# Optimization experiments

Measured on AMD Instinct MI355X. Metric: run time of the kernel, lower is better.

Reference implementation:

```python
import jax, jax.numpy as jnp
import numpy as np

GAMMA = 4  # channel groups (s)


def setup_inputs() -> dict:
    key = jax.random.key(0)
    k1, k2, k3, k4 = jax.random.split(key, 4)
    b, w, n, c = 16, 128, 256, 128  # batch, windows, win_size, channels
    x = jax.random.normal(k1, (b, w, n, c), dtype=jnp.float32)
    att_std = 0.01
    attention_centers = att_std * jax.random.normal(k2, (GAMMA, 1), dtype=jnp.float32)
    attention_spreads = 1.0 + att_std * jax.random.normal(k3, (GAMMA, 1), dtype=jnp.float32)
    token_proj_n_bias = 0.01 * jax.random.normal(k4, (1, n, 1), dtype=jnp.float32)
    return {"x": x, "attention_centers": attention_centers,
            "attention_spreads": attention_spreads,
            "token_proj_n_bias": token_proj_n_bias}


def _rel_indices(n):
    idx = jnp.arange(n, dtype=jnp.float32)
    d = idx[None, :] - idx[:, None]          # (n, n)
    return jnp.stack([d, d * d], axis=-1)     # (n, n, 2): [indx, indx^2]


def reference(x, attention_centers, attention_spreads, token_proj_n_bias):
    b, w, n, c = x.shape
    s = attention_centers.shape[0]
    v = c // s
    # pos_proj = -1/2 * [-2*delta*inv_cov, inv_cov]  -> (s, 2)
    pos_proj = -0.5 * jnp.concatenate(
        [-2.0 * attention_centers * attention_spreads, attention_spreads], axis=-1)
    rel = _rel_indices(n)                                   # (n, n, 2)
    pos_score = jnp.einsum('mnd,sd->mns', rel, pos_proj)    # (m, n, s)
    posmap = jax.nn.softmax(pos_score, axis=1)              # softmax over n
    xr = x.reshape(b, w, n, v, s)
    out = jnp.einsum('mns,bwnvs->bwmvs', posmap, xr)        # contract tokens n
    out = out + token_proj_n_bias[None, :, :, :, None]       # (1,1,n,1,1) broadcast
    return out.reshape(b, w, n, c)
```

## Files before the change

kernel.cpp:

```cpp
#include <hip/hip_runtime.h>
#include <hip/hip_bf16.h>


#define N_TOK 256
#define C_CH  128
#define NV    32
#define HW    8
#define TAPS  17
#define PMPAD 18
#define MCHUNK 64
#define ROWS  (MCHUNK + 2*HW)
#define XFL4  (ROWS * NV)
#define PMFL4 (MCHUNK * PMPAD)

typedef const __attribute__((address_space(1))) void gvoid_t;
typedef __attribute__((address_space(3))) void       lvoid_t;

__global__ void pm_build_kernel(const float* __restrict__ centers,
                                const float* __restrict__ spreads,
                                float* __restrict__ pmb) {
    const int m    = blockIdx.x;
    const int lane = threadIdx.x;
    const int n    = m + lane - HW;
    const bool valid = (lane < TAPS) && ((unsigned)n < N_TOK);
    const float dd = (float)(lane - HW);

    float e[4];
#pragma unroll
    for (int s = 0; s < 4; ++s) {
        const float ctr = centers[s];
        const float spr = spreads[s];
        const float sc = (ctr * spr) * dd - 0.5f * spr * dd * dd;
        e[s] = valid ? expf(sc) : 0.0f;
    }
#pragma unroll
    for (int s = 0; s < 4; ++s) {
        float v = e[s];
#pragma unroll
        for (int off = 32; off; off >>= 1) v += __shfl_xor(v, off, 64);
        e[s] = e[s] / __shfl(v, 0, 64);
    }
    if (lane < PMPAD) {
        reinterpret_cast<float4*>(pmb)[m * PMPAD + lane] =
            make_float4(e[0], e[1], e[2], e[3]);
    }
}

__global__ __launch_bounds__(256, 2)
void pm_apply_kernel(const float* __restrict__ x,
                     const float* __restrict__ pmb,
                     const float* __restrict__ bias,
                     float* __restrict__ out) {
    const int m0   = blockIdx.x * MCHUNK;
    const int bw   = blockIdx.y;
    const int row0 = m0 - HW;
    const int tid  = threadIdx.x;

    __shared__ float4 lds_x[XFL4];
    __shared__ float4 lds_pm[PMFL4];

    const float* xb = x + (size_t)bw * (N_TOK * C_CH);

#pragma unroll
    for (int i = 0; i < XFL4 / 256; ++i) {
        const int idx = tid + i * 256;
        const int r = idx >> 5;
        const int v = idx & 31;
        int n = row0 + r;
        n = n < 0 ? 0 : (n > N_TOK - 1 ? N_TOK - 1 : n);
        __builtin_amdgcn_global_load_lds((gvoid_t*)(xb + n * C_CH + v * 4),
                                         (lvoid_t*)&lds_x[idx], 16, 0, 0);
    }
    {
        const float4* src = reinterpret_cast<const float4*>(pmb) + m0 * PMPAD;
#pragma unroll
        for (int i = 0; i < 5; ++i) {
            const int idx = tid + i * 256;
            if (idx < PMFL4) {
                __builtin_amdgcn_global_load_lds((gvoid_t*)(src + idx),
                                                 (lvoid_t*)&lds_pm[idx], 16, 0, 0);
            }
        }
    }
    __syncthreads();

    const int vg    = tid & 15;
    const int mslot = tid >> 4;
    const int mloc  = mslot * 4;
    const int mbase = m0 + mloc;
    const int c0 = vg, c1 = vg + 16;

    float4 acc[4][2];
#pragma unroll
    for (int mi = 0; mi < 4; ++mi) {
        const float bv = bias[mbase + mi];
        acc[mi][0] = make_float4(bv, bv, bv, bv);
        acc[mi][1] = acc[mi][0];
    }

#pragma unroll
    for (int nr = 0; nr < 20; ++nr) {
        const int rbase = (mloc + nr) * NV;
        const float4 x0 = lds_x[rbase + c0];
        const float4 x1 = lds_x[rbase + c1];
#pragma unroll
        for (int mi = 0; mi < 4; ++mi) {
            const int d = nr - mi;
            if (d >= 0 && d < TAPS) {
                const float4 p = lds_pm[(mloc + mi) * PMPAD + d];
                acc[mi][0].x += p.x * x0.x;
                acc[mi][0].y += p.y * x0.y;
                acc[mi][0].z += p.z * x0.z;
                acc[mi][0].w += p.w * x0.w;
                acc[mi][1].x += p.x * x1.x;
                acc[mi][1].y += p.y * x1.y;
                acc[mi][1].z += p.z * x1.z;
                acc[mi][1].w += p.w * x1.w;
            }
        }
    }

    float4* ob = reinterpret_cast<float4*>(out + (size_t)bw * (N_TOK * C_CH));
#pragma unroll
    for (int mi = 0; mi < 4; ++mi) {
        ob[(mbase + mi) * NV + c0] = acc[mi][0];
        ob[(mbase + mi) * NV + c1] = acc[mi][1];
    }
}

extern "C" void kernel_launch(void* const* d_in, const int* in_sizes, int n_in,
                              void* d_out, int out_size, void* d_ws, size_t ws_size,
                              hipStream_t stream) {
    const float* x       = (const float*)d_in[0];
    const float* centers = (const float*)d_in[1];
    const float* spreads = (const float*)d_in[2];
    const float* bias    = (const float*)d_in[3];
    float* out = (float*)d_out;
    float* pmb = (float*)d_ws;

    pm_build_kernel<<<dim3(N_TOK), dim3(64), 0, stream>>>(centers, spreads, pmb);

    const int n_bw = 16 * 128;
    pm_apply_kernel<<<dim3(N_TOK / MCHUNK, n_bw), dim3(256), 0, stream>>>(
        x, pmb, bias, out);
}
```

Baseline: 110.0 us.

## Use shared interior softmax weights in scalar registers; remap blocks for locality

Away from the sequence edges, every output token uses the same 17-tap softmax weights, so interior rows read one weight row from global memory into scalar registers instead of staging a per-row weight tile in shared memory. Only edge rows, whose windows are truncated, keep per-row weights, which they now read straight from global memory. Removing the weight tile cuts shared-memory use and LDS traffic, so occupancy is raised to 4 blocks per SM. The launch grid is flattened into one dimension and remapped with an interleaving that spreads consecutive blocks across the batch-window range. The price is a divergent edge path and higher register pressure from the 68 scalar weights.

```diff
diff --git a/kernel.cpp b/kernel.cpp
--- a/kernel.cpp
+++ b/kernel.cpp
@@ -11,7 +11,6 @@
 #define MCHUNK 64
 #define ROWS  (MCHUNK + 2*HW)
 #define XFL4  (ROWS * NV)
-#define PMFL4 (MCHUNK * PMPAD)
 
 typedef const __attribute__((address_space(1))) void gvoid_t;
 typedef __attribute__((address_space(3))) void       lvoid_t;
@@ -46,18 +45,20 @@
     }
 }
 
-__global__ __launch_bounds__(256, 2)
+__global__ __launch_bounds__(256, 4)
 void pm_apply_kernel(const float* __restrict__ x,
                      const float* __restrict__ pmb,
                      const float* __restrict__ bias,
                      float* __restrict__ out) {
-    const int m0   = blockIdx.x * MCHUNK;
-    const int bw   = blockIdx.y;
-    const int row0 = m0 - HW;
-    const int tid  = threadIdx.x;
+    const int wid  = blockIdx.x;
+    const int work = (wid & 7) * 1024 + (wid >> 3);
+    const int chunk = work & 3;
+    const int bw    = work >> 2;
+    const int m0    = chunk * MCHUNK;
+    const int row0  = m0 - HW;
+    const int tid   = threadIdx.x;
 
     __shared__ float4 lds_x[XFL4];
-    __shared__ float4 lds_pm[PMFL4];
 
     const float* xb = x + (size_t)bw * (N_TOK * C_CH);
 
@@ -71,24 +72,22 @@
         __builtin_amdgcn_global_load_lds((gvoid_t*)(xb + n * C_CH + v * 4),
                                          (lvoid_t*)&lds_x[idx], 16, 0, 0);
     }
+
+    float wsc[TAPS * 4];
     {
-        const float4* src = reinterpret_cast<const float4*>(pmb) + m0 * PMPAD;
+        const float* wrow = pmb + 128 * (PMPAD * 4);
 #pragma unroll
-        for (int i = 0; i < 5; ++i) {
-            const int idx = tid + i * 256;
-            if (idx < PMFL4) {
-                __builtin_amdgcn_global_load_lds((gvoid_t*)(src + idx),
-                                                 (lvoid_t*)&lds_pm[idx], 16, 0, 0);
-            }
-        }
+        for (int t = 0; t < TAPS * 4; ++t)
+            wsc[t] = __int_as_float(
+                __builtin_amdgcn_readfirstlane(__float_as_int(wrow[t])));
     }
+
     __syncthreads();
 
     const int vg    = tid & 15;
     const int mslot = tid >> 4;
     const int mloc  = mslot * 4;
     const int mbase = m0 + mloc;
-    const int c0 = vg, c1 = vg + 16;
 
     float4 acc[4][2];
 #pragma unroll
@@ -98,24 +97,47 @@
         acc[mi][1] = acc[mi][0];
     }
 
+    const bool edge = (m0 == 0 && mslot < 2) || (m0 == 192 && mslot >= 14);
+    if (!edge) {
 #pragma unroll
-    for (int nr = 0; nr < 20; ++nr) {
-        const int rbase = (mloc + nr) * NV;
-        const float4 x0 = lds_x[rbase + c0];
-        const float4 x1 = lds_x[rbase + c1];
+        for (int nr = 0; nr < 20; ++nr) {
+            const int rbase = (mloc + nr) * NV;
+            const float4 x0 = lds_x[rbase + vg];
+            const float4 x1 = lds_x[rbase + vg + 16];
+#pragma unroll
+            for (int mi = 0; mi < 4; ++mi) {
+                const int d = nr - mi;
+                if (d >= 0 && d < TAPS) {
+                    acc[mi][0].x += wsc[d * 4 + 0] * x0.x;
+                    acc[mi][0].y += wsc[d * 4 + 1] * x0.y;
+                    acc[mi][0].z += wsc[d * 4 + 2] * x0.z;
+                    acc[mi][0].w += wsc[d * 4 + 3] * x0.w;
+                    acc[mi][1].x += wsc[d * 4 + 0] * x1.x;
+                    acc[mi][1].y += wsc[d * 4 + 1] * x1.y;
+                    acc[mi][1].z += wsc[d * 4 + 2] * x1.z;
+                    acc[mi][1].w += wsc[d * 4 + 3] * x1.w;
+                }
+            }
+        }
+    } else {
 #pragma unroll
         for (int mi = 0; mi < 4; ++mi) {
-            const int d = nr - mi;
-            if (d >= 0 && d < TAPS) {
-                const float4 p = lds_pm[(mloc + mi) * PMPAD + d];
-                acc[mi][0].x += p.x * x0.x;
-                acc[mi][0].y += p.y * x0.y;
-                acc[mi][0].z += p.z * x0.z;
-                acc[mi][0].w += p.w * x0.w;
-                acc[mi][1].x += p.x * x1.x;
-                acc[mi][1].y += p.y * x1.y;
-                acc[mi][1].z += p.z * x1.z;
-                acc[mi][1].w += p.w * x1.w;
+            const float4* pmrow =
+                reinterpret_cast<const float4*>(pmb) + (mbase + mi) * PMPAD;
+#pragma unroll
+            for (int t = 0; t < TAPS; ++t) {
+                const float4 w = pmrow[t];
+                const int rbase = (mloc + mi + t) * NV;
+                const float4 x0 = lds_x[rbase + vg];
+                const float4 x1 = lds_x[rbase + vg + 16];
+                acc[mi][0].x += w.x * x0.x;
+                acc[mi][0].y += w.y * x0.y;
+                acc[mi][0].z += w.z * x0.z;
+                acc[mi][0].w += w.w * x0.w;
+                acc[mi][1].x += w.x * x1.x;
+                acc[mi][1].y += w.y * x1.y;
+                acc[mi][1].z += w.z * x1.z;
+                acc[mi][1].w += w.w * x1.w;
             }
         }
     }
@@ -123,8 +145,8 @@
     float4* ob = reinterpret_cast<float4*>(out + (size_t)bw * (N_TOK * C_CH));
 #pragma unroll
     for (int mi = 0; mi < 4; ++mi) {
-        ob[(mbase + mi) * NV + c0] = acc[mi][0];
-        ob[(mbase + mi) * NV + c1] = acc[mi][1];
+        ob[(mbase + mi) * NV + vg] = acc[mi][0];
+        ob[(mbase + mi) * NV + vg + 16] = acc[mi][1];
     }
 }
 
@@ -140,7 +162,7 @@
 
     pm_build_kernel<<<dim3(N_TOK), dim3(64), 0, stream>>>(centers, spreads, pmb);
 
-    const int n_bw = 16 * 128;
-    pm_apply_kernel<<<dim3(N_TOK / MCHUNK, n_bw), dim3(256), 0, stream>>>(
+    const int n_blocks = (16 * 128) * (N_TOK / MCHUNK);
+    pm_apply_kernel<<<dim3(n_blocks), dim3(256), 0, stream>>>(
         x, pmb, bias, out);
 }
```

Result: slower. 253.0 us (+129.9%).
